# Kernel tuning notes

Hardware: AMD Instinct MI355X
Metric: run time of the kernel (lower is better)

## Reference

```python
import jax, jax.numpy as jnp
import numpy as np

N = 20000
E = 640000
D = 128
NORM_FACTOR = 100.0
LN_EPS = 1e-5


def _layer_norm(x, g, b):
    mu = jnp.mean(x, axis=-1, keepdims=True)
    var = jnp.var(x, axis=-1, keepdims=True)
    return (x - mu) * jax.lax.rsqrt(var + LN_EPS) * g + b


def setup_inputs() -> dict:
    key = jax.random.key(0)
    ks = jax.random.split(key, 16)

    def lin(k, fan_in, shape):
        bound = 1.0 / np.sqrt(fan_in)
        return jax.random.uniform(k, shape, jnp.float32, -bound, bound)

    h = jax.random.normal(ks[0], (N, D), jnp.float32)
    distances = jax.random.uniform(ks[1], (E, 1), jnp.float32)
    edges = jax.random.randint(ks[2], (2, E), 0, N, jnp.int64)
    node_mask = jnp.ones((N, 1), jnp.float32)
    edge_mask = jnp.ones((E, 1), jnp.float32)

    return {
        "h": h, "distances": distances, "node_mask": node_mask, "edge_mask": edge_mask,
        # linear: in->out
        "lin_w": lin(ks[3], D, (D, D)), "lin_b": lin(ks[4], D, (D,)),
        # att_mlp: (2D+1)->2D -> 2D->D -> D->1
        "att_w1": lin(ks[5], 2 * D + 1, (2 * D, 2 * D + 1)), "att_b1": lin(ks[5], 2 * D + 1, (2 * D,)),
        "att_w2": lin(ks[6], 2 * D, (D, 2 * D)), "att_b2": lin(ks[6], 2 * D, (D,)),
        "att_w3": lin(ks[7], D, (1, D)), "att_b3": lin(ks[7], D, (1,)),
        # node_mlp: D->D, LN, SiLU, D->D
        "nm_w1": lin(ks[8], D, (D, D)), "nm_b1": lin(ks[8], D, (D,)),
        "nm_ln_g": jnp.ones((D,), jnp.float32), "nm_ln_b": jnp.zeros((D,), jnp.float32),
        "nm_w2": lin(ks[9], D, (D, D)), "nm_b2": lin(ks[9], D, (D,)),
        # final LayerNorm
        "ln_g": jnp.ones((D,), jnp.float32), "ln_b": jnp.zeros((D,), jnp.float32),
        "edges": edges,
    }


def reference(h, distances, node_mask, edge_mask,
              lin_w, lin_b, att_w1, att_b1, att_w2, att_b2, att_w3, att_b3,
              nm_w1, nm_b1, nm_ln_g, nm_ln_b, nm_w2, nm_b2, ln_g, ln_b, edges):
    x = h @ lin_w.T + lin_b                                  # [N, D]
    row, col = edges[0], edges[1]
    x_row = x[row]                                           # [E, D]
    x_col = x[col]                                           # [E, D]

    # DenseAtt
    d = distances * edge_mask
    x_cat = jnp.concatenate([x_row, x_col, d], axis=1)       # [E, 2D+1]
    a = jax.nn.silu(x_cat @ att_w1.T + att_b1)
    a = jax.nn.silu(a @ att_w2.T + att_b2)
    att = jax.nn.sigmoid(a @ att_w3.T + att_b3) * edge_mask  # [E, 1]

    agg = x_col * att                                        # [E, D]
    out = jax.ops.segment_sum(agg, row, num_segments=N) / NORM_FACTOR

    # node_mlp + residual
    o = out @ nm_w1.T + nm_b1
    o = jax.nn.silu(_layer_norm(o, nm_ln_g, nm_ln_b))
    o = o @ nm_w2.T + nm_b2
    hh = o + x

    hh = _layer_norm(hh, ln_g, ln_b)
    hh = jax.nn.silu(hh)                                     # act = SiLU
    return hh
```

## Files before the change

kernel.cpp:

```cpp
#include <hip/hip_runtime.h>
#include <hip/hip_bf16.h>

#define N_NODES 20000
#define E_EDGES 640000
#define DIM 128
#define CAP 96
#define EPB 64
#define NPB 8
#define XST 264

typedef __attribute__((ext_vector_type(8))) short bf16x8;
typedef __attribute__((ext_vector_type(4))) float f32x4;

#define LOG2E 1.44269504f
__device__ __forceinline__ float fsilu(float x) {
    return x * __builtin_amdgcn_rcpf(1.f + __builtin_amdgcn_exp2f(-LOG2E * x));
}
__device__ __forceinline__ float fsig(float x) {
    return __builtin_amdgcn_rcpf(1.f + __builtin_amdgcn_exp2f(-LOG2E * x));
}

__device__ __forceinline__ unsigned short f2bf(float x) {
    union { float f; unsigned u; } v; v.f = x;
    unsigned r = (v.u + 0x7fffu + ((v.u >> 16) & 1u)) >> 16;
    return (unsigned short)r;
}
__device__ __forceinline__ float bf2f(unsigned short s) {
    union { unsigned u; float f; } v; v.u = ((unsigned)s) << 16;
    return v.f;
}
__device__ __forceinline__ unsigned pack_bf16(float lo, float hi) {
    union { float f; unsigned u; } a, b; a.f = lo; b.f = hi;
    unsigned ul = a.u + 0x8000u, uh = b.u + 0x8000u;
    return __builtin_amdgcn_perm(uh, ul, 0x07060302u);
}

#define PRE_PREP_BLOCKS 64
#define PRE_LIN_BLOCKS  625
#define PRE_ADJ_BLOCKS  2500
__global__ __launch_bounds__(256) void pre_kernel(
    const float* __restrict__ w1, const float* __restrict__ w2,
    unsigned short* __restrict__ w1b, float* __restrict__ w1p,
    unsigned short* __restrict__ w2b,
    const float* __restrict__ h, const float* __restrict__ lw,
    const float* __restrict__ lb, float* __restrict__ x,
    unsigned short* __restrict__ xb,
    const int* __restrict__ edges, int* __restrict__ cnt,
    int2* __restrict__ adj2, int E) {
    __shared__ float hs[32][128];
    int b = blockIdx.x;
    int t = threadIdx.x;

    if (b < PRE_PREP_BLOCKS) {
        int i = b * 256 + t;
        const int stride = PRE_PREP_BLOCKS * 256;
        for (int idx = i; idx < 256 * 256; idx += stride) {
            int o = idx >> 8, k = idx & 255;
            w1b[idx] = f2bf(w1[o * 257 + k]);
        }
        for (int idx = i; idx < 128 * 256; idx += stride) {
            int n2 = idx >> 8, p = idx & 255;
            int bb = p & ~31, off = p & 31;
            int ksrc = bb + (off >> 1) + ((off & 1) << 4);
            w2b[idx] = f2bf(w2[n2 * 256 + ksrc]);
        }
        for (int idx = i; idx < 256; idx += stride) {
            int bb = idx & ~31, off = idx & 31;
            int ksrc = bb + (off >> 1) + ((off & 1) << 4);
            w1p[idx] = w1[ksrc * 257 + 256];
        }
    } else if (b < PRE_PREP_BLOCKS + PRE_LIN_BLOCKS) {
        int nb = b - PRE_PREP_BLOCKS;
        int n0 = nb * 32;
        int ch = t & 127, g = t >> 7;
#pragma unroll
        for (int j = 0; j < 16; ++j) hs[g * 16 + j][ch] = h[(size_t)(n0 + g * 16 + j) * DIM + ch];
        __syncthreads();
        float acc[16];
#pragma unroll
        for (int j = 0; j < 16; ++j) acc[j] = 0.f;
        for (int kc = 0; kc < 128; kc += 4) {
            float4 wv = *(const float4*)&lw[(size_t)ch * DIM + kc];
#pragma unroll
            for (int j = 0; j < 16; ++j)
                acc[j] += wv.x * hs[g * 16 + j][kc] + wv.y * hs[g * 16 + j][kc + 1]
                        + wv.z * hs[g * 16 + j][kc + 2] + wv.w * hs[g * 16 + j][kc + 3];
        }
        float bias = lb[ch];
#pragma unroll
        for (int j = 0; j < 16; ++j) {
            float v = acc[j] + bias;
            int n = n0 + g * 16 + j;
            x[(size_t)n * DIM + ch] = v;
            xb[(size_t)n * DIM + ch] = f2bf(v);
        }
    } else {
        int e = (b - PRE_PREP_BLOCKS - PRE_LIN_BLOCKS) * 256 + t;
        if (e < E) {
            int r = edges[e];
            int col = edges[E + e];
            int slot = atomicAdd(&cnt[r], 1);
            if (slot < CAP) { int2 v; v.x = e; v.y = col; adj2[(size_t)r * CAP + slot] = v; }
        }
    }
}

#define PRC_NPB 16
__global__ __launch_bounds__(256) void prc_kernel(
    const unsigned short* __restrict__ xb,
    const unsigned short* __restrict__ w1b,
    const float* __restrict__ b1,
    unsigned short* __restrict__ pr, unsigned short* __restrict__ pc) {
    int n0 = blockIdx.x * PRC_NPB;
    int w = threadIdx.x >> 6, lane = threadIdx.x & 63;
    int lrow = lane & 15, quad = lane >> 4;

    bf16x8 a[4];
#pragma unroll
    for (int kk = 0; kk < 4; ++kk)
        a[kk] = *(const bf16x8*)&xb[(size_t)(n0 + lrow) * DIM + kk * 32 + quad * 8];

    f32x4 z = {0.f, 0.f, 0.f, 0.f};
#pragma unroll
    for (int i = 0; i < 8; ++i) {
        int gt = w * 8 + i;
        int half = gt >> 4;
        int obase = (gt & 15) * 16;
        f32x4 acc = z;
#pragma unroll
        for (int kk = 0; kk < 4; ++kk) {
            bf16x8 bfrag = *(const bf16x8*)&w1b[(size_t)(obase + lrow) * 256 + half * 128 + kk * 32 + quad * 8];
            acc = __builtin_amdgcn_mfma_f32_16x16x32_bf16(a[kk], bfrag, acc, 0, 0, 0);
        }
        int o = obase + lrow;
        float bias = half ? 0.f : b1[o];
        unsigned short* dst = half ? pc : pr;
#pragma unroll
        for (int r = 0; r < 4; ++r)
            dst[(size_t)(n0 + quad * 4 + r) * 256 + o] = f2bf(acc[r] + bias);
    }
}

__global__ __launch_bounds__(512, 4) void edge_kernel(
    const unsigned short* __restrict__ pr, const unsigned short* __restrict__ pc,
    const float* __restrict__ dist, const float* __restrict__ emask,
    const int* __restrict__ edges,
    const float* __restrict__ w1p,
    const unsigned short* __restrict__ w2b, const float* __restrict__ b2,
    const float* __restrict__ w3, const float* __restrict__ b3v,
    float* __restrict__ att, int E) {
    __shared__ unsigned short buf[EPB * XST];
    __shared__ float part[8][EPB];
    __shared__ float w1ps[256];
    __shared__ float dvals[EPB];
    __shared__ int ridx[EPB], cidx[EPB];

    int tid = threadIdx.x;
    int eb = blockIdx.x * EPB;

    if (tid < EPB) {
        int e = eb + tid;
        ridx[tid] = edges[e];
        cidx[tid] = edges[E + e];
        dvals[tid] = dist[e] * emask[e];
    }
    if (tid >= 64 && tid < 320) w1ps[tid - 64] = w1p[tid - 64];

    int wave = tid >> 6, lane = tid & 63;
    int lrow = lane & 15, quad = lane >> 4;
    int n2 = wave * 16 + lrow;
    float bias2 = b2[n2];
    float w3v = w3[n2];

    __syncthreads();

    {
        int ge = tid >> 3, cb = tid & 7;
        size_t rbase = (size_t)ridx[ge] * 256 + cb * 32;
        size_t cbase = (size_t)cidx[ge] * 256 + cb * 32;
        float d = dvals[ge];
        unsigned* wrow = (unsigned*)&buf[ge * XST + cb * 32];
        const float* wp = &w1ps[cb * 32];

        bf16x8 pA = *(const bf16x8*)&pr[rbase];
        bf16x8 pB = *(const bf16x8*)&pr[rbase + 16];
        bf16x8 qA = *(const bf16x8*)&pc[cbase];
        bf16x8 qB = *(const bf16x8*)&pc[cbase + 16];
#pragma unroll
        for (int l = 0; l < 8; ++l) {
            float s0 = bf2f((unsigned short)pA[l]) + bf2f((unsigned short)qA[l]) + d * wp[2 * l];
            float s1 = bf2f((unsigned short)pB[l]) + bf2f((unsigned short)qB[l]) + d * wp[2 * l + 1];
            wrow[l] = pack_bf16(fsilu(s0), fsilu(s1));
        }
        pA = *(const bf16x8*)&pr[rbase + 8];
        pB = *(const bf16x8*)&pr[rbase + 24];
        qA = *(const bf16x8*)&pc[cbase + 8];
        qB = *(const bf16x8*)&pc[cbase + 24];
#pragma unroll
        for (int l = 0; l < 8; ++l) {
            float s0 = bf2f((unsigned short)pA[l]) + bf2f((unsigned short)qA[l]) + d * wp[16 + 2 * l];
            float s1 = bf2f((unsigned short)pB[l]) + bf2f((unsigned short)qB[l]) + d * wp[16 + 2 * l + 1];
            wrow[8 + l] = pack_bf16(fsilu(s0), fsilu(s1));
        }
    }
    __syncthreads();

    f32x4 zz = {0.f, 0.f, 0.f, 0.f};
    f32x4 acc2[4];
#pragma unroll
    for (int mt = 0; mt < 4; ++mt) acc2[mt] = zz;

    for (int kk = 0; kk < 8; ++kk) {
        int ka = kk * 32 + quad * 8;
        bf16x8 bfrag = *(const bf16x8*)&w2b[(size_t)n2 * 256 + ka];
#pragma unroll
        for (int mt = 0; mt < 4; ++mt) {
            bf16x8 a = *(bf16x8*)&buf[(mt * 16 + lrow) * XST + ka];
            acc2[mt] = __builtin_amdgcn_mfma_f32_16x16x32_bf16(a, bfrag, acc2[mt], 0, 0, 0);
        }
    }

    float s[4][4];
#pragma unroll
    for (int mt = 0; mt < 4; ++mt)
#pragma unroll
        for (int r = 0; r < 4; ++r)
            s[mt][r] = fsilu(acc2[mt][r] + bias2) * w3v;
#pragma unroll
    for (int off = 1; off < 16; off <<= 1) {
#pragma unroll
        for (int mt = 0; mt < 4; ++mt)
#pragma unroll
            for (int r = 0; r < 4; ++r)
                s[mt][r] += __shfl_xor(s[mt][r], off);
    }
    if (lrow == 0) {
#pragma unroll
        for (int mt = 0; mt < 4; ++mt)
#pragma unroll
            for (int r = 0; r < 4; ++r)
                part[wave][mt * 16 + quad * 4 + r] = s[mt][r];
    }
    __syncthreads();

    if (tid < EPB) {
        float ssum = b3v[0];
#pragma unroll
        for (int w = 0; w < 8; ++w) ssum += part[w][tid];
        att[eb + tid] = fsig(ssum) * emask[eb + tid];
    }
}

__global__ __launch_bounds__(256) void node_kernel(
    const float* __restrict__ attv, const int2* __restrict__ adj2, const int* __restrict__ cnt,
    const unsigned short* __restrict__ xb,
    const float* __restrict__ x,
    const float* __restrict__ w1, const float* __restrict__ bb1,
    const float* __restrict__ lng, const float* __restrict__ lnb,
    const float* __restrict__ w2, const float* __restrict__ bb2,
    const float* __restrict__ gF, const float* __restrict__ bF,
    float* __restrict__ out, int E) {
    __shared__ float atts[NPB][CAP];
    __shared__ int   cols[NPB][CAP];
    __shared__ float outv[NPB][128];
    __shared__ float bufs[NPB][128];
    __shared__ float mu_s[NPB], rs_s[NPB];
    __shared__ int cnts[NPB];

    int t = threadIdx.x;
    int n0 = blockIdx.x * NPB;

    if (t < NPB) { int c = cnt[n0 + t]; cnts[t] = c > CAP ? CAP : c; }
    __syncthreads();

    {
        int jg = t >> 5, l = t & 31;
        int c = cnts[jg];
        const int2* al = adj2 + (size_t)(n0 + jg) * CAP;
        for (int i = l; i < c; i += 32) {
            int2 v = al[i];
            atts[jg][i] = attv[v.x];
            cols[jg][i] = v.y;
        }
    }
    __syncthreads();

    int w = t >> 6, lane = t & 63;
#pragma unroll
    for (int jj = 0; jj < 2; ++jj) {
        int j = w * 2 + jj;
        int c = cnts[j];
        float lo0 = 0.f, hi0 = 0.f, lo1 = 0.f, hi1 = 0.f;
        float lo2 = 0.f, hi2 = 0.f, lo3 = 0.f, hi3 = 0.f;
        int i = 0;
        for (; i + 3 < c; i += 4) {
            unsigned u0 = *(const unsigned*)&xb[(size_t)cols[j][i]     * DIM + lane * 2];
            unsigned u1 = *(const unsigned*)&xb[(size_t)cols[j][i + 1] * DIM + lane * 2];
            unsigned u2 = *(const unsigned*)&xb[(size_t)cols[j][i + 2] * DIM + lane * 2];
            unsigned u3 = *(const unsigned*)&xb[(size_t)cols[j][i + 3] * DIM + lane * 2];
            float w0 = atts[j][i], w1v = atts[j][i + 1], w2v = atts[j][i + 2], w3v = atts[j][i + 3];
            lo0 += w0 * bf2f((unsigned short)(u0 & 0xffff)); hi0 += w0 * bf2f((unsigned short)(u0 >> 16));
            lo1 += w1v * bf2f((unsigned short)(u1 & 0xffff)); hi1 += w1v * bf2f((unsigned short)(u1 >> 16));
            lo2 += w2v * bf2f((unsigned short)(u2 & 0xffff)); hi2 += w2v * bf2f((unsigned short)(u2 >> 16));
            lo3 += w3v * bf2f((unsigned short)(u3 & 0xffff)); hi3 += w3v * bf2f((unsigned short)(u3 >> 16));
        }
        for (; i < c; ++i) {
            unsigned u0 = *(const unsigned*)&xb[(size_t)cols[j][i] * DIM + lane * 2];
            float w0 = atts[j][i];
            lo0 += w0 * bf2f((unsigned short)(u0 & 0xffff));
            hi0 += w0 * bf2f((unsigned short)(u0 >> 16));
        }
        outv[j][lane * 2]     = ((lo0 + lo1) + (lo2 + lo3)) * 0.01f;
        outv[j][lane * 2 + 1] = ((hi0 + hi1) + (hi2 + hi3)) * 0.01f;
    }
    __syncthreads();

    int h = t >> 7, ch = t & 127;
    float xres[4];
#pragma unroll
    for (int jj = 0; jj < 4; ++jj)
        xres[jj] = x[(size_t)(n0 + h * 4 + jj) * DIM + ch];

    float a1[4] = {0, 0, 0, 0};
    for (int kc = 0; kc < 128; kc += 4) {
        float4 wv = *(const float4*)&w1[(size_t)ch * DIM + kc];
#pragma unroll
        for (int jj = 0; jj < 4; ++jj) {
            int j = h * 4 + jj;
            a1[jj] += wv.x * outv[j][kc] + wv.y * outv[j][kc + 1] + wv.z * outv[j][kc + 2] + wv.w * outv[j][kc + 3];
        }
    }
    float bias1 = bb1[ch];
#pragma unroll
    for (int jj = 0; jj < 4; ++jj) bufs[h * 4 + jj][ch] = a1[jj] + bias1;
    __syncthreads();

    {
        int j = t >> 5, l = t & 31;
        float s = 0.f, qq = 0.f;
#pragma unroll
        for (int i = 0; i < 4; ++i) { float v = bufs[j][l + 32 * i]; s += v; qq += v * v; }
#pragma unroll
        for (int off = 16; off; off >>= 1) { s += __shfl_xor(s, off); qq += __shfl_xor(qq, off); }
        if (l == 0) {
            float mu = s * (1.f / 128.f);
            float var = qq * (1.f / 128.f) - mu * mu;
            mu_s[j] = mu; rs_s[j] = __builtin_amdgcn_rsqf(var + 1e-5f);
        }
    }
    __syncthreads();

    float g = lng[ch], bb = lnb[ch];
    float h2[4];
#pragma unroll
    for (int jj = 0; jj < 4; ++jj) {
        int j = h * 4 + jj;
        h2[jj] = fsilu((bufs[j][ch] - mu_s[j]) * rs_s[j] * g + bb);
    }
    __syncthreads();
#pragma unroll
    for (int jj = 0; jj < 4; ++jj) bufs[h * 4 + jj][ch] = h2[jj];
    __syncthreads();

    float a3[4] = {0, 0, 0, 0};
    for (int kc = 0; kc < 128; kc += 4) {
        float4 wv = *(const float4*)&w2[(size_t)ch * DIM + kc];
#pragma unroll
        for (int jj = 0; jj < 4; ++jj) {
            int j = h * 4 + jj;
            a3[jj] += wv.x * bufs[j][kc] + wv.y * bufs[j][kc + 1] + wv.z * bufs[j][kc + 2] + wv.w * bufs[j][kc + 3];
        }
    }
    float bias2 = bb2[ch];
    float hh[4];
#pragma unroll
    for (int jj = 0; jj < 4; ++jj) hh[jj] = a3[jj] + bias2 + xres[jj];
    __syncthreads();
#pragma unroll
    for (int jj = 0; jj < 4; ++jj) bufs[h * 4 + jj][ch] = hh[jj];
    __syncthreads();

    {
        int j = t >> 5, l = t & 31;
        float s = 0.f, qq = 0.f;
#pragma unroll
        for (int i = 0; i < 4; ++i) { float v = bufs[j][l + 32 * i]; s += v; qq += v * v; }
#pragma unroll
        for (int off = 16; off; off >>= 1) { s += __shfl_xor(s, off); qq += __shfl_xor(qq, off); }
        if (l == 0) {
            float mu = s * (1.f / 128.f);
            float var = qq * (1.f / 128.f) - mu * mu;
            mu_s[j] = mu; rs_s[j] = __builtin_amdgcn_rsqf(var + 1e-5f);
        }
    }
    __syncthreads();

    float gf = gF[ch], bf = bF[ch];
#pragma unroll
    for (int jj = 0; jj < 4; ++jj) {
        int j = h * 4 + jj;
        float y = (hh[jj] - mu_s[j]) * rs_s[j] * gf + bf;
        out[(size_t)(n0 + j) * DIM + ch] = fsilu(y);
    }
}

extern "C" void kernel_launch(void* const* d_in, const int* in_sizes, int n_in,
                              void* d_out, int out_size, void* d_ws, size_t ws_size,
                              hipStream_t stream) {
    const float* h         = (const float*)d_in[0];
    const float* distances = (const float*)d_in[1];
    const float* edge_mask = (const float*)d_in[3];
    const float* lin_w     = (const float*)d_in[4];
    const float* lin_b     = (const float*)d_in[5];
    const float* att_w1    = (const float*)d_in[6];
    const float* att_b1    = (const float*)d_in[7];
    const float* att_w2    = (const float*)d_in[8];
    const float* att_b2    = (const float*)d_in[9];
    const float* att_w3    = (const float*)d_in[10];
    const float* att_b3    = (const float*)d_in[11];
    const float* nm_w1     = (const float*)d_in[12];
    const float* nm_b1     = (const float*)d_in[13];
    const float* nm_ln_g   = (const float*)d_in[14];
    const float* nm_ln_b   = (const float*)d_in[15];
    const float* nm_w2     = (const float*)d_in[16];
    const float* nm_b2     = (const float*)d_in[17];
    const float* ln_g      = (const float*)d_in[18];
    const float* ln_b      = (const float*)d_in[19];
    const int*   edges     = (const int*)d_in[20];
    float* out = (float*)d_out;

    const int N = N_NODES, E = E_EDGES;

    char* ws = (char*)d_ws;
    float* x            = (float*)ws;            ws += (size_t)N * DIM * 4;
    unsigned short* xb  = (unsigned short*)ws;   ws += (size_t)N * DIM * 2;
    float* attv         = (float*)ws;            ws += (size_t)E * 4;
    int* cnt            = (int*)ws;              ws += (size_t)N * 4;
    int2* adj2          = (int2*)ws;             ws += (size_t)N * CAP * 8;
    unsigned short* w1b = (unsigned short*)ws;   ws += 256 * 256 * 2;
    float* w1p          = (float*)ws;            ws += 256 * 4;
    unsigned short* w2b = (unsigned short*)ws;   ws += 128 * 256 * 2;
    unsigned short* pr  = (unsigned short*)ws;   ws += (size_t)N * 256 * 2;
    unsigned short* pc  = (unsigned short*)ws;   ws += (size_t)N * 256 * 2;

    hipMemsetAsync(cnt, 0, (size_t)N * 4, stream);

    pre_kernel<<<PRE_PREP_BLOCKS + PRE_LIN_BLOCKS + PRE_ADJ_BLOCKS, 256, 0, stream>>>(
        att_w1, att_w2, w1b, w1p, w2b,
        h, lin_w, lin_b, x, xb,
        edges, cnt, adj2, E);
    prc_kernel<<<N / PRC_NPB, 256, 0, stream>>>(xb, w1b, att_b1, pr, pc);
    edge_kernel<<<E / EPB, 512, 0, stream>>>(pr, pc, distances, edge_mask, edges,
                                             w1p, w2b, att_b2,
                                             att_w3, att_b3, attv, E);
    node_kernel<<<N / NPB, 256, 0, stream>>>(attv, adj2, cnt, xb, x,
                                             nm_w1, nm_b1, nm_ln_g, nm_ln_b,
                                             nm_w2, nm_b2, ln_g, ln_b, out, E);
}
```

Baseline: 398.9 us.

## Process edges grouped by destination node using CSR adjacency in edge kernel

The edge kernel now iterates over the per-node adjacency lists built in the pre kernel instead of raw edge order, so each block handles 8 destination nodes. Row projections come from a small set of rows that stay in cache, and the row half of the first-layer projection is stored as fp32. Distance and mask are packed into the adjacency during the pre pass, and attention is written in adjacency order, so the node kernel drops its indirect gather through edge ids. In exchange, tiles can be partly empty because node degrees vary, each tile needs extra shared-memory staging, and the fp32 row buffer is larger.

```diff
diff --git a/kernel.cpp b/kernel.cpp
--- a/kernel.cpp
+++ b/kernel.cpp
@@ -45,8 +45,10 @@
     const float* __restrict__ h, const float* __restrict__ lw,
     const float* __restrict__ lb, float* __restrict__ x,
     unsigned short* __restrict__ xb,
-    const int* __restrict__ edges, int* __restrict__ cnt,
-    int2* __restrict__ adj2, int E) {
+    const int* __restrict__ edges,
+    const float* __restrict__ dist, const float* __restrict__ emask,
+    int* __restrict__ cnt,
+    int* __restrict__ adjc, float2* __restrict__ dm, int E) {
     __shared__ float hs[32][128];
     int b = blockIdx.x;
     int t = threadIdx.x;
@@ -100,7 +102,12 @@
             int r = edges[e];
             int col = edges[E + e];
             int slot = atomicAdd(&cnt[r], 1);
-            if (slot < CAP) { int2 v; v.x = e; v.y = col; adj2[(size_t)r * CAP + slot] = v; }
+            if (slot < CAP) {
+                adjc[(size_t)r * CAP + slot] = col;
+                float em = emask[e];
+                float2 de; de.x = dist[e] * em; de.y = em;
+                dm[(size_t)r * CAP + slot] = de;
+            }
         }
     }
 }
@@ -110,7 +117,7 @@
     const unsigned short* __restrict__ xb,
     const unsigned short* __restrict__ w1b,
     const float* __restrict__ b1,
-    unsigned short* __restrict__ pr, unsigned short* __restrict__ pc) {
+    float* __restrict__ prf, unsigned short* __restrict__ pcb) {
     int n0 = blockIdx.x * PRC_NPB;
     int w = threadIdx.x >> 6, lane = threadIdx.x & 63;
     int lrow = lane & 15, quad = lane >> 4;
@@ -133,126 +140,175 @@
             acc = __builtin_amdgcn_mfma_f32_16x16x32_bf16(a[kk], bfrag, acc, 0, 0, 0);
         }
         int o = obase + lrow;
-        float bias = half ? 0.f : b1[o];
-        unsigned short* dst = half ? pc : pr;
-#pragma unroll
-        for (int r = 0; r < 4; ++r)
-            dst[(size_t)(n0 + quad * 4 + r) * 256 + o] = f2bf(acc[r] + bias);
+        if (half == 0) {
+            float bias = b1[o];
+#pragma unroll
+            for (int r = 0; r < 4; ++r)
+                prf[(size_t)(n0 + quad * 4 + r) * 256 + o] = acc[r] + bias;
+        } else {
+#pragma unroll
+            for (int r = 0; r < 4; ++r)
+                pcb[(size_t)(n0 + quad * 4 + r) * 256 + o] = f2bf(acc[r]);
+        }
     }
 }
 
 __global__ __launch_bounds__(512, 4) void edge_kernel(
-    const unsigned short* __restrict__ pr, const unsigned short* __restrict__ pc,
-    const float* __restrict__ dist, const float* __restrict__ emask,
-    const int* __restrict__ edges,
+    const float* __restrict__ prf, const unsigned short* __restrict__ pcb,
+    const float2* __restrict__ dm, const int* __restrict__ adjc,
+    const int* __restrict__ cnt,
     const float* __restrict__ w1p,
     const unsigned short* __restrict__ w2b, const float* __restrict__ b2,
     const float* __restrict__ w3, const float* __restrict__ b3v,
-    float* __restrict__ att, int E) {
+    float* __restrict__ attA) {
     __shared__ unsigned short buf[EPB * XST];
     __shared__ float part[8][EPB];
     __shared__ float w1ps[256];
-    __shared__ float dvals[EPB];
-    __shared__ int ridx[EPB], cidx[EPB];
+    __shared__ unsigned short list[NPB * CAP];
+    __shared__ int offs[NPB + 1];
+    __shared__ int cnts[NPB];
+    __shared__ int cidx_s[EPB], jj_s[EPB];
+    __shared__ float dv_s[EPB], em_s[EPB];
 
     int tid = threadIdx.x;
-    int eb = blockIdx.x * EPB;
-
-    if (tid < EPB) {
-        int e = eb + tid;
-        ridx[tid] = edges[e];
-        cidx[tid] = edges[E + e];
-        dvals[tid] = dist[e] * emask[e];
-    }
-    if (tid >= 64 && tid < 320) w1ps[tid - 64] = w1p[tid - 64];
+    int n0 = blockIdx.x * NPB;
+
+    if (tid < NPB) { int c = cnt[n0 + tid]; cnts[tid] = c > CAP ? CAP : c; }
+    if (tid >= 256 && tid < 512) w1ps[tid - 256] = w1p[tid - 256];
+    __syncthreads();
+    if (tid == 0) {
+        int s = 0;
+#pragma unroll
+        for (int j = 0; j < NPB; ++j) { offs[j] = s; s += cnts[j]; }
+        offs[NPB] = s;
+    }
+    __syncthreads();
+    {
+        int jg = tid >> 5, l = tid & 31;
+        if (jg < NPB) {
+            int c = cnts[jg], o = offs[jg];
+            for (int i = l; i < c; i += 32) list[o + i] = (unsigned short)((jg << 8) | i);
+        }
+    }
+    int count = offs[NPB];
+    int ntiles = (count + EPB - 1) / EPB;
+    __syncthreads();
 
     int wave = tid >> 6, lane = tid & 63;
     int lrow = lane & 15, quad = lane >> 4;
     int n2 = wave * 16 + lrow;
     float bias2 = b2[n2];
     float w3v = w3[n2];
-
-    __syncthreads();
-
-    {
-        int ge = tid >> 3, cb = tid & 7;
-        size_t rbase = (size_t)ridx[ge] * 256 + cb * 32;
-        size_t cbase = (size_t)cidx[ge] * 256 + cb * 32;
-        float d = dvals[ge];
-        unsigned* wrow = (unsigned*)&buf[ge * XST + cb * 32];
-        const float* wp = &w1ps[cb * 32];
-
-        bf16x8 pA = *(const bf16x8*)&pr[rbase];
-        bf16x8 pB = *(const bf16x8*)&pr[rbase + 16];
-        bf16x8 qA = *(const bf16x8*)&pc[cbase];
-        bf16x8 qB = *(const bf16x8*)&pc[cbase + 16];
-#pragma unroll
-        for (int l = 0; l < 8; ++l) {
-            float s0 = bf2f((unsigned short)pA[l]) + bf2f((unsigned short)qA[l]) + d * wp[2 * l];
-            float s1 = bf2f((unsigned short)pB[l]) + bf2f((unsigned short)qB[l]) + d * wp[2 * l + 1];
-            wrow[l] = pack_bf16(fsilu(s0), fsilu(s1));
-        }
-        pA = *(const bf16x8*)&pr[rbase + 8];
-        pB = *(const bf16x8*)&pr[rbase + 24];
-        qA = *(const bf16x8*)&pc[cbase + 8];
-        qB = *(const bf16x8*)&pc[cbase + 24];
-#pragma unroll
-        for (int l = 0; l < 8; ++l) {
-            float s0 = bf2f((unsigned short)pA[l]) + bf2f((unsigned short)qA[l]) + d * wp[16 + 2 * l];
-            float s1 = bf2f((unsigned short)pB[l]) + bf2f((unsigned short)qB[l]) + d * wp[16 + 2 * l + 1];
-            wrow[8 + l] = pack_bf16(fsilu(s0), fsilu(s1));
-        }
-    }
-    __syncthreads();
+    float b3s = b3v[0];
 
     f32x4 zz = {0.f, 0.f, 0.f, 0.f};
-    f32x4 acc2[4];
-#pragma unroll
-    for (int mt = 0; mt < 4; ++mt) acc2[mt] = zz;
-
-    for (int kk = 0; kk < 8; ++kk) {
-        int ka = kk * 32 + quad * 8;
-        bf16x8 bfrag = *(const bf16x8*)&w2b[(size_t)n2 * 256 + ka];
-#pragma unroll
-        for (int mt = 0; mt < 4; ++mt) {
-            bf16x8 a = *(bf16x8*)&buf[(mt * 16 + lrow) * XST + ka];
-            acc2[mt] = __builtin_amdgcn_mfma_f32_16x16x32_bf16(a, bfrag, acc2[mt], 0, 0, 0);
-        }
-    }
-
-    float s[4][4];
-#pragma unroll
-    for (int mt = 0; mt < 4; ++mt)
-#pragma unroll
-        for (int r = 0; r < 4; ++r)
-            s[mt][r] = fsilu(acc2[mt][r] + bias2) * w3v;
-#pragma unroll
-    for (int off = 1; off < 16; off <<= 1) {
+
+    for (int t = 0; t < ntiles; ++t) {
+        if (tid < EPB) {
+            int s = t * EPB + tid;
+            if (s < count) {
+                int ji = list[s];
+                int j = ji >> 8, i = ji & 255;
+                size_t ai = (size_t)(n0 + j) * CAP + i;
+                float2 de = dm[ai];
+                jj_s[tid] = j; cidx_s[tid] = adjc[ai];
+                dv_s[tid] = de.x; em_s[tid] = de.y;
+            } else {
+                jj_s[tid] = 0; cidx_s[tid] = 0;
+                dv_s[tid] = 0.f; em_s[tid] = 0.f;
+            }
+        }
+        __syncthreads();
+
+        {
+            int ge = tid >> 3, cb = tid & 7;
+            const unsigned short* pcp = pcb + (size_t)cidx_s[ge] * 256 + cb * 32;
+            const float* prow = prf + (size_t)(n0 + jj_s[ge]) * 256 + cb * 32;
+            float d = dv_s[ge];
+            unsigned* wrow = (unsigned*)&buf[ge * XST + cb * 32];
+            const float* wp = &w1ps[cb * 32];
+
+            float pa[8], pb[8];
+            *(float4*)&pa[0] = *(const float4*)&prow[0];
+            *(float4*)&pa[4] = *(const float4*)&prow[4];
+            *(float4*)&pb[0] = *(const float4*)&prow[16];
+            *(float4*)&pb[4] = *(const float4*)&prow[20];
+            bf16x8 qA = *(const bf16x8*)&pcp[0];
+            bf16x8 qB = *(const bf16x8*)&pcp[16];
+#pragma unroll
+            for (int l = 0; l < 8; ++l) {
+                float s0 = pa[l] + bf2f((unsigned short)qA[l]) + d * wp[2 * l];
+                float s1 = pb[l] + bf2f((unsigned short)qB[l]) + d * wp[2 * l + 1];
+                wrow[l] = pack_bf16(fsilu(s0), fsilu(s1));
+            }
+            *(float4*)&pa[0] = *(const float4*)&prow[8];
+            *(float4*)&pa[4] = *(const float4*)&prow[12];
+            *(float4*)&pb[0] = *(const float4*)&prow[24];
+            *(float4*)&pb[4] = *(const float4*)&prow[28];
+            qA = *(const bf16x8*)&pcp[8];
+            qB = *(const bf16x8*)&pcp[24];
+#pragma unroll
+            for (int l = 0; l < 8; ++l) {
+                float s0 = pa[l] + bf2f((unsigned short)qA[l]) + d * wp[16 + 2 * l];
+                float s1 = pb[l] + bf2f((unsigned short)qB[l]) + d * wp[16 + 2 * l + 1];
+                wrow[8 + l] = pack_bf16(fsilu(s0), fsilu(s1));
+            }
+        }
+        __syncthreads();
+
+        f32x4 acc2[4];
+#pragma unroll
+        for (int mt = 0; mt < 4; ++mt) acc2[mt] = zz;
+
+        for (int kk = 0; kk < 8; ++kk) {
+            int ka = kk * 32 + quad * 8;
+            bf16x8 bfrag = *(const bf16x8*)&w2b[(size_t)n2 * 256 + ka];
+#pragma unroll
+            for (int mt = 0; mt < 4; ++mt) {
+                bf16x8 a = *(bf16x8*)&buf[(mt * 16 + lrow) * XST + ka];
+                acc2[mt] = __builtin_amdgcn_mfma_f32_16x16x32_bf16(a, bfrag, acc2[mt], 0, 0, 0);
+            }
+        }
+
+        float s[4][4];
 #pragma unroll
         for (int mt = 0; mt < 4; ++mt)
 #pragma unroll
             for (int r = 0; r < 4; ++r)
-                s[mt][r] += __shfl_xor(s[mt][r], off);
-    }
-    if (lrow == 0) {
-#pragma unroll
-        for (int mt = 0; mt < 4; ++mt)
-#pragma unroll
-            for (int r = 0; r < 4; ++r)
-                part[wave][mt * 16 + quad * 4 + r] = s[mt][r];
-    }
-    __syncthreads();
-
-    if (tid < EPB) {
-        float ssum = b3v[0];
-#pragma unroll
-        for (int w = 0; w < 8; ++w) ssum += part[w][tid];
-        att[eb + tid] = fsig(ssum) * emask[eb + tid];
+                s[mt][r] = fsilu(acc2[mt][r] + bias2) * w3v;
+#pragma unroll
+        for (int off = 1; off < 16; off <<= 1) {
+#pragma unroll
+            for (int mt = 0; mt < 4; ++mt)
+#pragma unroll
+                for (int r = 0; r < 4; ++r)
+                    s[mt][r] += __shfl_xor(s[mt][r], off);
+        }
+        if (lrow == 0) {
+#pragma unroll
+            for (int mt = 0; mt < 4; ++mt)
+#pragma unroll
+                for (int r = 0; r < 4; ++r)
+                    part[wave][mt * 16 + quad * 4 + r] = s[mt][r];
+        }
+        __syncthreads();
+
+        if (tid < EPB) {
+            int sidx = t * EPB + tid;
+            if (sidx < count) {
+                float ssum = b3s;
+#pragma unroll
+                for (int w = 0; w < 8; ++w) ssum += part[w][tid];
+                int ji = list[sidx];
+                int j = ji >> 8, i = ji & 255;
+                attA[(size_t)(n0 + j) * CAP + i] = fsig(ssum) * em_s[tid];
+            }
+        }
     }
 }
 
 __global__ __launch_bounds__(256) void node_kernel(
-    const float* __restrict__ attv, const int2* __restrict__ adj2, const int* __restrict__ cnt,
+    const float* __restrict__ attA, const int* __restrict__ adjc, const int* __restrict__ cnt,
     const unsigned short* __restrict__ xb,
     const float* __restrict__ x,
     const float* __restrict__ w1, const float* __restrict__ bb1,
@@ -276,11 +332,11 @@
     {
         int jg = t >> 5, l = t & 31;
         int c = cnts[jg];
-        const int2* al = adj2 + (size_t)(n0 + jg) * CAP;
+        const int* al = adjc + (size_t)(n0 + jg) * CAP;
+        const float* av = attA + (size_t)(n0 + jg) * CAP;
         for (int i = l; i < c; i += 32) {
-            int2 v = al[i];
-            atts[jg][i] = attv[v.x];
-            cols[jg][i] = v.y;
+            atts[jg][i] = av[i];
+            cols[jg][i] = al[i];
         }
     }
     __syncthreads();
@@ -434,26 +490,27 @@
     char* ws = (char*)d_ws;
     float* x            = (float*)ws;            ws += (size_t)N * DIM * 4;
     unsigned short* xb  = (unsigned short*)ws;   ws += (size_t)N * DIM * 2;
-    float* attv         = (float*)ws;            ws += (size_t)E * 4;
     int* cnt            = (int*)ws;              ws += (size_t)N * 4;
-    int2* adj2          = (int2*)ws;             ws += (size_t)N * CAP * 8;
+    int* adjc           = (int*)ws;              ws += (size_t)N * CAP * 4;
+    float2* dm          = (float2*)ws;           ws += (size_t)N * CAP * 8;
+    float* attA         = (float*)ws;            ws += (size_t)N * CAP * 4;
     unsigned short* w1b = (unsigned short*)ws;   ws += 256 * 256 * 2;
     float* w1p          = (float*)ws;            ws += 256 * 4;
     unsigned short* w2b = (unsigned short*)ws;   ws += 128 * 256 * 2;
-    unsigned short* pr  = (unsigned short*)ws;   ws += (size_t)N * 256 * 2;
-    unsigned short* pc  = (unsigned short*)ws;   ws += (size_t)N * 256 * 2;
+    float* prf          = (float*)ws;            ws += (size_t)N * 256 * 4;
+    unsigned short* pcb = (unsigned short*)ws;   ws += (size_t)N * 256 * 2;
 
     hipMemsetAsync(cnt, 0, (size_t)N * 4, stream);
 
     pre_kernel<<<PRE_PREP_BLOCKS + PRE_LIN_BLOCKS + PRE_ADJ_BLOCKS, 256, 0, stream>>>(
         att_w1, att_w2, w1b, w1p, w2b,
         h, lin_w, lin_b, x, xb,
-        edges, cnt, adj2, E);
-    prc_kernel<<<N / PRC_NPB, 256, 0, stream>>>(xb, w1b, att_b1, pr, pc);
-    edge_kernel<<<E / EPB, 512, 0, stream>>>(pr, pc, distances, edge_mask, edges,
+        edges, distances, edge_mask, cnt, adjc, dm, E);
+    prc_kernel<<<N / PRC_NPB, 256, 0, stream>>>(xb, w1b, att_b1, prf, pcb);
+    edge_kernel<<<N / NPB, 512, 0, stream>>>(prf, pcb, dm, adjc, cnt,
                                              w1p, w2b, att_b2,
-                                             att_w3, att_b3, attv, E);
-    node_kernel<<<N / NPB, 256, 0, stream>>>(attv, adj2, cnt, xb, x,
+                                             att_w3, att_b3, attA);
+    node_kernel<<<N / NPB, 256, 0, stream>>>(attA, adjc, cnt, xb, x,
                                              nm_w1, nm_b1, nm_ln_g, nm_ln_b,
                                              nm_w2, nm_b2, ln_g, ln_b, out, E);
 }
```

New measurement: 478.9 us. 1.2x slower.
